# Performance work log

Measured on AMD Instinct MI355X. Metric: run time of the kernel, lower is better.

Reference implementation:

```python
import jax, jax.numpy as jnp
import numpy as np

DIM = 256
HEADS = 8
HEAD_DIM = DIM // HEADS
WS = (2, 8, 8)  # window size (t, h, w)
N = WS[0] * WS[1] * WS[2]  # 128 tokens per window
SCALE = HEAD_DIM ** -0.5
MLP_HIDDEN = int(DIM * 2.0)
EPS = 1e-5

# static relative-position index table [N, N]
def _rel_pos_index():
    coords = np.stack(np.meshgrid(np.arange(WS[0]), np.arange(WS[1]), np.arange(WS[2]), indexing='ij'))
    cf = coords.reshape(3, -1)
    rel = cf[:, :, None] - cf[:, None, :]
    rel = rel.transpose(1, 2, 0).copy()
    rel[..., 0] += WS[0] - 1
    rel[..., 1] += WS[1] - 1
    rel[..., 2] += WS[2] - 1
    rel[..., 0] *= (2 * WS[1] - 1) * (2 * WS[2] - 1)
    rel[..., 1] *= (2 * WS[2] - 1)
    return rel.sum(-1)

REL_IDX = jnp.asarray(_rel_pos_index())  # [N, N] int
TABLE_SIZE = (2 * WS[0] - 1) * (2 * WS[1] - 1) * (2 * WS[2] - 1)  # 675


def layernorm(x, g, b):
    m = jnp.mean(x, axis=-1, keepdims=True)
    var = jnp.mean(jnp.square(x - m), axis=-1, keepdims=True)
    return (x - m) * jax.lax.rsqrt(var + EPS) * g + b


def window_partition(x):
    B, T, H, W, C = x.shape
    x = x.reshape(B, T // WS[0], WS[0], H // WS[1], WS[1], W // WS[2], WS[2], C)
    x = x.transpose(0, 1, 3, 5, 2, 4, 6, 7)
    return x.reshape(-1, N, C)


def window_reverse(wins, B, T, H, W):
    C = wins.shape[-1]
    x = wins.reshape(B, T // WS[0], H // WS[1], W // WS[2], WS[0], WS[1], WS[2], C)
    x = x.transpose(0, 1, 4, 2, 5, 3, 6, 7)
    return x.reshape(B, T, H, W, C)


def setup_inputs() -> dict:
    key = jax.random.key(0)
    ks = jax.random.split(key, 20)
    B, T, H, W = 2, 8, 64, 64
    f = lambda k, s, sc=0.02: jax.random.normal(k, s, dtype=jnp.float32) * sc
    return {
        'q': jax.random.normal(ks[0], (B, T, H, W, DIM), dtype=jnp.float32),
        'k': jax.random.normal(ks[1], (B, T, H, W, DIM), dtype=jnp.float32),
        'v': jax.random.normal(ks[2], (B, T, H, W, DIM), dtype=jnp.float32),
        'gq': jnp.ones((DIM,), jnp.float32), 'bq': jnp.zeros((DIM,), jnp.float32),
        'gk': jnp.ones((DIM,), jnp.float32), 'bk': jnp.zeros((DIM,), jnp.float32),
        'gv': jnp.ones((DIM,), jnp.float32), 'bv': jnp.zeros((DIM,), jnp.float32),
        'bias_table': f(ks[3], (TABLE_SIZE, HEADS)),
        'proj_w': f(ks[4], (DIM, DIM)), 'proj_b': jnp.zeros((DIM,), jnp.float32),
        'g2': jnp.ones((DIM,), jnp.float32), 'b2': jnp.zeros((DIM,), jnp.float32),
        'mw1': f(ks[5], (MLP_HIDDEN, DIM)), 'mb1': jnp.zeros((MLP_HIDDEN,), jnp.float32),
        'mw2': f(ks[6], (DIM, MLP_HIDDEN)), 'mb2': jnp.zeros((DIM,), jnp.float32),
    }


def reference(q, k, v, gq, bq, gk, bk, gv, bv, bias_table, proj_w, proj_b, g2, b2, mw1, mb1, mw2, mb2):
    B, T, H, W, C = q.shape
    shortcut = v
    qn = layernorm(q, gq, bq)
    kn = layernorm(k, gk, bk)
    vn = layernorm(v, gv, bv)
    # (dims divisible by window -> no padding needed)
    qw = window_partition(qn)  # [B_, N, C]
    kw = window_partition(kn)
    vw = window_partition(vn)
    B_ = qw.shape[0]
    to_heads = lambda t: t.reshape(B_, N, HEADS, HEAD_DIM).transpose(0, 2, 1, 3)  # [B_, h, N, d]
    qh, kh, vh = to_heads(qw), to_heads(kw), to_heads(vw)
    attn = jnp.einsum('bhnd,bhmd->bhnm', qh * SCALE, kh)
    bias = bias_table[REL_IDX]  # [N, N, heads]
    attn = attn + bias.transpose(2, 0, 1)[None]
    attn = jax.nn.softmax(attn, axis=-1)
    out = jnp.einsum('bhnm,bhmd->bhnd', attn, vh)
    out = out.transpose(0, 2, 1, 3).reshape(B_, N, C)
    out = out @ proj_w.T + proj_b
    x = window_reverse(out, B, T, H, W)
    x = shortcut + x
    h1 = layernorm(x, g2, b2)
    h1 = jax.nn.gelu(h1 @ mw1.T + mb1, approximate=False)
    x = x + (h1 @ mw2.T + mb2)
    return x
```

## Files before the change

### kernel.cpp

```cpp
#include <hip/hip_runtime.h>
#include <math.h>


typedef __attribute__((ext_vector_type(8))) short short8;
typedef __attribute__((ext_vector_type(4))) short shortx4;
typedef __attribute__((ext_vector_type(4))) float floatx4;

#define MFMA16(a, b, c) __builtin_amdgcn_mfma_f32_16x16x32_bf16((a), (b), (c), 0, 0, 0)
#define ATT_SCALE 0.17677669529663689f

__device__ __forceinline__ short f2bf(float f) {
  unsigned u = __float_as_uint(f);
  u += 0x7fffu + ((u >> 16) & 1u);
  return (short)(u >> 16);
}
__device__ __forceinline__ float bf2f(short s) {
  return __uint_as_float(((unsigned)(unsigned short)s) << 16);
}
__device__ __forceinline__ void gl2lds(const short* g, short* l) {
  __builtin_amdgcn_global_load_lds((const __attribute__((address_space(1))) void*)(g),
                                   (__attribute__((address_space(3))) void*)(l), 16, 0, 0);
}

__global__ void cvt_kernel(const float* __restrict__ src, short* __restrict__ dst, int n) {
  int i = blockIdx.x * 256 + threadIdx.x;
  if (i < n) dst[i] = f2bf(src[i]);
}

__global__ void biasprep_kernel(const float* __restrict__ table, short* __restrict__ biasPb) {
  int idx = blockIdx.x * 256 + threadIdx.x;
  int h = idx >> 14;
  int n = (idx >> 7) & 127;
  int lr = (idx >> 3) & 15;
  int c = idx & 7;
  int m = 16 * c + lr;
  int t1 = n >> 6, h1 = (n >> 3) & 7, w1 = n & 7;
  int t2 = m >> 6, h2 = (m >> 3) & 7, w2 = m & 7;
  int ridx = (t1 - t2 + 1) * 225 + (h1 - h2 + 7) * 15 + (w1 - w2 + 7);
  biasPb[idx] = f2bf(table[ridx * 8 + h]);
}

__global__ __launch_bounds__(256) void stats_kernel(
    const float* __restrict__ q, const float* __restrict__ k, const float* __restrict__ v,
    float2* __restrict__ sq, float2* __restrict__ sk, float2* __restrict__ sv) {
  const int wv = threadIdx.x >> 6, l = threadIdx.x & 63;
  const int tok = blockIdx.x * 4 + wv;
  const int which = blockIdx.y;
  const float* src = (which == 0) ? q : ((which == 1) ? k : v);
  float2* dst = (which == 0) ? sq : ((which == 1) ? sk : sv);
  float4 xv = *(const float4*)(src + (size_t)tok * 256 + l * 4);
  float s1 = xv.x + xv.y + xv.z + xv.w;
  float s2 = xv.x * xv.x + xv.y * xv.y + xv.z * xv.z + xv.w * xv.w;
#pragma unroll
  for (int off = 1; off < 64; off <<= 1) {
    s1 += __shfl_xor(s1, off);
    s2 += __shfl_xor(s2, off);
  }
  float mean = s1 * (1.0f / 256.0f);
  float var = s2 * (1.0f / 256.0f) - mean * mean;
  if (l == 0) dst[tok] = make_float2(mean, rsqrtf(var + 1e-5f));
}

__global__ __launch_bounds__(256, 4) void attn_kernel(
    const float* __restrict__ q, const float* __restrict__ k, const float* __restrict__ v,
    const float* __restrict__ gq, const float* __restrict__ bq,
    const float* __restrict__ gk, const float* __restrict__ bk,
    const float* __restrict__ gv, const float* __restrict__ bv,
    const float2* __restrict__ sq, const float2* __restrict__ sk, const float2* __restrict__ sv,
    const short* __restrict__ biasPb, short* __restrict__ ao) {
  __shared__ union SU {
    struct { short Qs[128][40]; short Ks[128][40]; } qk;
    short Ps[128 * 128];
  } su;
  __shared__ short Vt[32 * 128];

  const int wi = blockIdx.x, h = blockIdx.y, tid = threadIdx.x;
  const int b_ = wi >> 8, tt = (wi >> 6) & 3, hb = (wi >> 3) & 7, wb = wi & 7;
  const int uu = tid & 7;

  const float4 gq4 = *(const float4*)(gq + h * 32 + uu * 4);
  const float4 bq4 = *(const float4*)(bq + h * 32 + uu * 4);
  const float4 gk4 = *(const float4*)(gk + h * 32 + uu * 4);
  const float4 bk4 = *(const float4*)(bk + h * 32 + uu * 4);
  const float4 gv4 = *(const float4*)(gv + h * 32 + uu * 4);
  const float4 bv4 = *(const float4*)(bv + h * 32 + uu * 4);

#pragma unroll
  for (int p = 0; p < 4; ++p) {
    int row = p * 32 + (tid >> 3);
    int t = row >> 6, h2 = (row >> 3) & 7, w2 = row & 7;
    size_t sidx = (((size_t)(b_ * 8 + tt * 2 + t)) * 64 + hb * 8 + h2) * 64 + wb * 8 + w2;
    size_t gbase = sidx * 256 + h * 32 + uu * 4;
    {
      float4 xv = *(const float4*)(q + gbase);
      float2 st = sq[sidx];
      shortx4 o;
      o[0] = f2bf((xv.x - st.x) * st.y * gq4.x + bq4.x);
      o[1] = f2bf((xv.y - st.x) * st.y * gq4.y + bq4.y);
      o[2] = f2bf((xv.z - st.x) * st.y * gq4.z + bq4.z);
      o[3] = f2bf((xv.w - st.x) * st.y * gq4.w + bq4.w);
      *(shortx4*)&su.qk.Qs[row][uu * 4] = o;
    }
    {
      float4 xv = *(const float4*)(k + gbase);
      float2 st = sk[sidx];
      shortx4 o;
      o[0] = f2bf((xv.x - st.x) * st.y * gk4.x + bk4.x);
      o[1] = f2bf((xv.y - st.x) * st.y * gk4.y + bk4.y);
      o[2] = f2bf((xv.z - st.x) * st.y * gk4.z + bk4.z);
      o[3] = f2bf((xv.w - st.x) * st.y * gk4.w + bk4.w);
      *(shortx4*)&su.qk.Ks[row][uu * 4] = o;
    }
    {
      float4 xv = *(const float4*)(v + gbase);
      float2 st = sv[sidx];
      float vals[4] = {(xv.x - st.x) * st.y * gv4.x + bv4.x,
                       (xv.y - st.x) * st.y * gv4.y + bv4.y,
                       (xv.z - st.x) * st.y * gv4.z + bv4.z,
                       (xv.w - st.x) * st.y * gv4.w + bv4.w};
#pragma unroll
      for (int e = 0; e < 4; ++e) {
        int d = uu * 4 + e;
        Vt[d * 128 + (((row >> 3) ^ (d & 7)) << 3) + (row & 7)] = f2bf(vals[e]);
      }
    }
  }
  __syncthreads();

  const int wvv = tid >> 6, l = tid & 63, lr = l & 15, g = l >> 4;
  const floatx4 zf = {0.f, 0.f, 0.f, 0.f};

  short8 aq0 = *(const short8*)&su.qk.Qs[32 * wvv + lr][g * 8];
  short8 aq1 = *(const short8*)&su.qk.Qs[32 * wvv + 16 + lr][g * 8];

  floatx4 s[2][8];
#pragma unroll
  for (int c = 0; c < 8; ++c) {
    short8 bk8 = *(const short8*)&su.qk.Ks[16 * c + lr][g * 8];
    s[0][c] = MFMA16(aq0, bk8, zf);
    s[1][c] = MFMA16(aq1, bk8, zf);
  }
  __syncthreads();

  const int lr7 = lr & 7;
#pragma unroll
  for (int r = 0; r < 2; ++r) {
#pragma unroll
    for (int j = 0; j < 4; ++j) {
      int n = 32 * wvv + 16 * r + 4 * g + j;
      short8 bv8 = *(const short8*)(biasPb + ((size_t)(h * 128 + n) * 16 + lr) * 8);
      float mx = -1e30f;
#pragma unroll
      for (int c = 0; c < 8; ++c) {
        float val = s[r][c][j] * ATT_SCALE + bf2f(bv8[c]);
        s[r][c][j] = val;
        mx = fmaxf(mx, val);
      }
#pragma unroll
      for (int off = 1; off < 16; off <<= 1) mx = fmaxf(mx, __shfl_xor(mx, off));
      float sum = 0.f;
#pragma unroll
      for (int c = 0; c < 8; ++c) {
        float e = __expf(s[r][c][j] - mx);
        s[r][c][j] = e;
        sum += e;
      }
#pragma unroll
      for (int off = 1; off < 16; off <<= 1) sum += __shfl_xor(sum, off);
      float invs = 1.0f / sum;
      int n7 = n & 7;
#pragma unroll
      for (int c = 0; c < 8; ++c) {
        int col = 16 * c + lr;
        su.Ps[n * 128 + (((col >> 3) ^ n7) << 3) + (col & 7)] = f2bf(s[r][c][j] * invs);
      }
    }
  }

  floatx4 o00 = zf, o01 = zf, o10 = zf, o11 = zf;
  const int ra0 = 32 * wvv + lr, ra1 = ra0 + 16;
#pragma unroll
  for (int ks = 0; ks < 4; ++ks) {
    int ulog = ks * 4 + g;
    short8 pa0 = *(const short8*)&su.Ps[ra0 * 128 + ((ulog ^ (ra0 & 7)) << 3)];
    short8 pa1 = *(const short8*)&su.Ps[ra1 * 128 + ((ulog ^ (ra1 & 7)) << 3)];
    short8 vb0 = *(const short8*)&Vt[lr * 128 + ((ulog ^ lr7) << 3)];
    short8 vb1 = *(const short8*)&Vt[(16 + lr) * 128 + ((ulog ^ lr7) << 3)];
    o00 = MFMA16(pa0, vb0, o00);
    o01 = MFMA16(pa0, vb1, o01);
    o10 = MFMA16(pa1, vb0, o10);
    o11 = MFMA16(pa1, vb1, o11);
  }
#pragma unroll
  for (int j = 0; j < 4; ++j) {
    int n0 = 32 * wvv + 4 * g + j;
    int n1 = n0 + 16;
    size_t rb0 = ((size_t)wi * 128 + n0) * 256 + h * 32;
    size_t rb1 = ((size_t)wi * 128 + n1) * 256 + h * 32;
    ao[rb0 + lr] = f2bf(o00[j]);
    ao[rb0 + 16 + lr] = f2bf(o01[j]);
    ao[rb1 + lr] = f2bf(o10[j]);
    ao[rb1 + 16 + lr] = f2bf(o11[j]);
  }
}

template <int K>
__device__ __forceinline__ void gemm_core(const short* __restrict__ A,
                                          const short* __restrict__ W,
                                          floatx4 (&acc)[16]) {
  __shared__ short As[128 * 64];
  __shared__ short Ws[256 * 64];
  const int tid = threadIdx.x;
  const int w = tid >> 6, l = tid & 63, lr = l & 15, g = l >> 4;
  const floatx4 zf = {0.f, 0.f, 0.f, 0.f};
#pragma unroll
  for (int i = 0; i < 16; ++i) acc[i] = zf;

  const int li = l >> 3, u = l & 7;
  const int swz = ((u ^ li) << 3);
  const size_t aoff0 = (size_t)(w * 8 + li) * K + swz;
  const size_t aoff1 = (size_t)((w + 8) * 8 + li) * K + swz;
  const size_t woff0 = (size_t)(w * 8 + li) * K + swz;
  const size_t woff1 = (size_t)((w + 8) * 8 + li) * K + swz;
  const size_t woff2 = (size_t)((w + 16) * 8 + li) * K + swz;
  const size_t woff3 = (size_t)((w + 24) * 8 + li) * K + swz;
  short* dA0 = As + w * 512;
  short* dA1 = As + (w + 8) * 512;
  short* dW0 = Ws + w * 512;
  short* dW1 = Ws + (w + 8) * 512;
  short* dW2 = Ws + (w + 16) * 512;
  short* dW3 = Ws + (w + 24) * 512;

  const int ra = 16 * w + lr;
  const int s0 = ((g ^ (lr & 7)) << 3);
  const int s1 = (((4 + g) ^ (lr & 7)) << 3);

  for (int k0 = 0; k0 < K; k0 += 64) {
    if (k0) __syncthreads();
    gl2lds(A + aoff0 + k0, dA0);
    gl2lds(A + aoff1 + k0, dA1);
    gl2lds(W + woff0 + k0, dW0);
    gl2lds(W + woff1 + k0, dW1);
    gl2lds(W + woff2 + k0, dW2);
    gl2lds(W + woff3 + k0, dW3);
    __syncthreads();
    short8 a0 = *(const short8*)&As[ra * 64 + s0];
    short8 a1 = *(const short8*)&As[ra * 64 + s1];
#pragma unroll
    for (int ct = 0; ct < 16; ++ct) {
      int rb = ct * 16 + lr;
      short8 b0 = *(const short8*)&Ws[rb * 64 + s0];
      acc[ct] = MFMA16(a0, b0, acc[ct]);
      short8 b1 = *(const short8*)&Ws[rb * 64 + s1];
      acc[ct] = MFMA16(a1, b1, acc[ct]);
    }
  }
}

__global__ __launch_bounds__(512, 4) void proj_kernel(
    const short* __restrict__ ao, const short* __restrict__ wp,
    const float* __restrict__ proj_b, const float* __restrict__ vin,
    const float* __restrict__ g2, const float* __restrict__ b2,
    float* __restrict__ x, short* __restrict__ xln) {
  floatx4 acc[16];
  gemm_core<256>(ao + (size_t)blockIdx.x * 128 * 256, wp, acc);
  const int tid = threadIdx.x, w = tid >> 6, l = tid & 63, lr = l & 15, g = l >> 4;
#pragma unroll
  for (int j = 0; j < 4; ++j) {
    int mrow = blockIdx.x * 128 + 16 * w + 4 * g + j;
    int wi = mrow >> 7, n = mrow & 127;
    int wb = wi & 7, hb = (wi >> 3) & 7, tt = (wi >> 6) & 3, b_ = wi >> 8;
    int t = tt * 2 + (n >> 6), hh = hb * 8 + ((n >> 3) & 7), ww = wb * 8 + (n & 7);
    size_t sidx = (((size_t)b_ * 8 + t) * 64 + hh) * 64 + ww;
    float xr[16];
    float ss1 = 0.f, ss2 = 0.f;
#pragma unroll
    for (int ct = 0; ct < 16; ++ct) {
      int col = ct * 16 + lr;
      float val = acc[ct][j] + proj_b[col] + vin[sidx * 256 + col];
      xr[ct] = val;
      ss1 += val;
      ss2 += val * val;
    }
#pragma unroll
    for (int off = 1; off < 16; off <<= 1) {
      ss1 += __shfl_xor(ss1, off);
      ss2 += __shfl_xor(ss2, off);
    }
    float mean = ss1 * (1.0f / 256.0f);
    float var = ss2 * (1.0f / 256.0f) - mean * mean;
    float inv = rsqrtf(var + 1e-5f);
#pragma unroll
    for (int ct = 0; ct < 16; ++ct) {
      int col = ct * 16 + lr;
      x[sidx * 256 + col] = xr[ct];
      xln[sidx * 256 + col] = f2bf((xr[ct] - mean) * inv * g2[col] + b2[col]);
    }
  }
}

__global__ __launch_bounds__(512, 4) void mlp1_kernel(
    const short* __restrict__ xln, const short* __restrict__ w1,
    const float* __restrict__ mb1, short* __restrict__ h1) {
  floatx4 acc[16];
  gemm_core<256>(xln + (size_t)blockIdx.x * 128 * 256, w1 + (size_t)blockIdx.y * 256 * 256, acc);
  const int tid = threadIdx.x, w = tid >> 6, l = tid & 63, lr = l & 15, g = l >> 4;
  const int colbase = blockIdx.y * 256;
#pragma unroll
  for (int ct = 0; ct < 16; ++ct) {
    int col = ct * 16 + lr;
    float bias = mb1[colbase + col];
#pragma unroll
    for (int j = 0; j < 4; ++j) {
      int mrow = blockIdx.x * 128 + 16 * w + 4 * g + j;
      float val = acc[ct][j] + bias;
      float ge = 0.5f * val * (1.0f + erff(val * 0.70710678118654752f));
      h1[(size_t)mrow * 512 + colbase + col] = f2bf(ge);
    }
  }
}

__global__ __launch_bounds__(512, 4) void mlp2_kernel(
    const short* __restrict__ h1, const short* __restrict__ w2,
    const float* __restrict__ mb2, const float* __restrict__ x,
    float* __restrict__ out) {
  floatx4 acc[16];
  gemm_core<512>(h1 + (size_t)blockIdx.x * 128 * 512, w2, acc);
  const int tid = threadIdx.x, w = tid >> 6, l = tid & 63, lr = l & 15, g = l >> 4;
#pragma unroll
  for (int ct = 0; ct < 16; ++ct) {
    int col = ct * 16 + lr;
    float bias = mb2[col];
#pragma unroll
    for (int j = 0; j < 4; ++j) {
      int mrow = blockIdx.x * 128 + 16 * w + 4 * g + j;
      out[(size_t)mrow * 256 + col] = x[(size_t)mrow * 256 + col] + acc[ct][j] + bias;
    }
  }
}

extern "C" void kernel_launch(void* const* d_in, const int* in_sizes, int n_in,
                              void* d_out, int out_size, void* d_ws, size_t ws_size,
                              hipStream_t stream) {
  const float* q = (const float*)d_in[0];
  const float* k = (const float*)d_in[1];
  const float* v = (const float*)d_in[2];
  const float* gq = (const float*)d_in[3];
  const float* bq = (const float*)d_in[4];
  const float* gk = (const float*)d_in[5];
  const float* bk = (const float*)d_in[6];
  const float* gv = (const float*)d_in[7];
  const float* bv = (const float*)d_in[8];
  const float* bias_table = (const float*)d_in[9];
  const float* proj_w = (const float*)d_in[10];
  const float* proj_b = (const float*)d_in[11];
  const float* g2 = (const float*)d_in[12];
  const float* b2 = (const float*)d_in[13];
  const float* mw1 = (const float*)d_in[14];
  const float* mb1 = (const float*)d_in[15];
  const float* mw2 = (const float*)d_in[16];
  const float* mb2 = (const float*)d_in[17];

  char* ws = (char*)d_ws;
  float2* sq = (float2*)(ws + 0);
  float2* sk = (float2*)(ws + 524288);
  float2* sv = (float2*)(ws + 1048576);
  float* x = (float*)(ws + 0);
  short* ao = (short*)(ws + 67108864);
  short* h1 = (short*)(ws + 67108864);
  short* xln = (short*)(ws + 134217728);
  short* wp = (short*)(ws + 167772160);
  short* w1 = (short*)(ws + 167903232);
  short* w2 = (short*)(ws + 168165376);
  short* biasPb = (short*)(ws + 168427520);

  cvt_kernel<<<256, 256, 0, stream>>>(proj_w, wp, 65536);
  cvt_kernel<<<512, 256, 0, stream>>>(mw1, w1, 131072);
  cvt_kernel<<<512, 256, 0, stream>>>(mw2, w2, 131072);
  biasprep_kernel<<<512, 256, 0, stream>>>(bias_table, biasPb);

  stats_kernel<<<dim3(16384, 3), 256, 0, stream>>>(q, k, v, sq, sk, sv);

  attn_kernel<<<dim3(512, 8), 256, 0, stream>>>(q, k, v, gq, bq, gk, bk, gv, bv,
                                                sq, sk, sv, biasPb, ao);

  proj_kernel<<<512, 512, 0, stream>>>(ao, wp, proj_b, v, g2, b2, x, xln);

  mlp1_kernel<<<dim3(512, 2), 512, 0, stream>>>(xln, w1, mb1, h1);

  mlp2_kernel<<<512, 512, 0, stream>>>(h1, w2, mb2, x, (float*)d_out);
}
```

Baseline: 249.5 us.

## Precompute windowed bf16 LayerNorm QKV and fuse proj+MLP into one kernel

The stats kernel now applies LayerNorm fully and writes bf16 Q/K/V already in window-partitioned order, so the attention kernel only copies contiguous bf16 tiles instead of re-reading fp32 inputs with per-head strided gathers. The projection, residual, second LayerNorm, MLP1 with GELU and MLP2 are fused into one kernel over 64-row tiles. It keeps the LN output and hidden activations in LDS and the residual in registers, which removes the global round trips for x, xln and h1. In exchange it uses heavier register and LDS use per block at lower occupancy, and reloads weights per 64-row tile.

New measurement: 236.8 us. -5.1%, faster.

```diff
diff --git a/kernel.cpp b/kernel.cpp
--- a/kernel.cpp
+++ b/kernel.cpp
@@ -40,14 +40,20 @@
   biasPb[idx] = f2bf(table[ridx * 8 + h]);
 }
 
-__global__ __launch_bounds__(256) void stats_kernel(
+__global__ __launch_bounds__(256) void ln_qkv_kernel(
     const float* __restrict__ q, const float* __restrict__ k, const float* __restrict__ v,
-    float2* __restrict__ sq, float2* __restrict__ sk, float2* __restrict__ sv) {
+    const float* __restrict__ gq, const float* __restrict__ bq,
+    const float* __restrict__ gk, const float* __restrict__ bk,
+    const float* __restrict__ gv, const float* __restrict__ bv,
+    short* __restrict__ qw, short* __restrict__ kw, short* __restrict__ vw) {
   const int wv = threadIdx.x >> 6, l = threadIdx.x & 63;
   const int tok = blockIdx.x * 4 + wv;
   const int which = blockIdx.y;
   const float* src = (which == 0) ? q : ((which == 1) ? k : v);
-  float2* dst = (which == 0) ? sq : ((which == 1) ? sk : sv);
+  const float* gg  = (which == 0) ? gq : ((which == 1) ? gk : gv);
+  const float* bb  = (which == 0) ? bq : ((which == 1) ? bk : bv);
+  short* dst       = (which == 0) ? qw : ((which == 1) ? kw : vw);
+
   float4 xv = *(const float4*)(src + (size_t)tok * 256 + l * 4);
   float s1 = xv.x + xv.y + xv.z + xv.w;
   float s2 = xv.x * xv.x + xv.y * xv.y + xv.z * xv.z + xv.w * xv.w;
@@ -58,15 +64,25 @@
   }
   float mean = s1 * (1.0f / 256.0f);
   float var = s2 * (1.0f / 256.0f) - mean * mean;
-  if (l == 0) dst[tok] = make_float2(mean, rsqrtf(var + 1e-5f));
+  float inv = rsqrtf(var + 1e-5f);
+
+  int b_ = tok >> 15, rem = tok & 32767;
+  int t = rem >> 12, hh = (rem >> 6) & 63, ww = rem & 63;
+  int wi = ((b_ * 4 + (t >> 1)) * 8 + (hh >> 3)) * 8 + (ww >> 3);
+  int n = ((t & 1) << 6) | ((hh & 7) << 3) | (ww & 7);
+
+  float4 g4 = *(const float4*)(gg + l * 4);
+  float4 b4 = *(const float4*)(bb + l * 4);
+  shortx4 o;
+  o[0] = f2bf((xv.x - mean) * inv * g4.x + b4.x);
+  o[1] = f2bf((xv.y - mean) * inv * g4.y + b4.y);
+  o[2] = f2bf((xv.z - mean) * inv * g4.z + b4.z);
+  o[3] = f2bf((xv.w - mean) * inv * g4.w + b4.w);
+  *(shortx4*)(dst + ((size_t)wi * 128 + n) * 256 + l * 4) = o;
 }
 
 __global__ __launch_bounds__(256, 4) void attn_kernel(
-    const float* __restrict__ q, const float* __restrict__ k, const float* __restrict__ v,
-    const float* __restrict__ gq, const float* __restrict__ bq,
-    const float* __restrict__ gk, const float* __restrict__ bk,
-    const float* __restrict__ gv, const float* __restrict__ bv,
-    const float2* __restrict__ sq, const float2* __restrict__ sk, const float2* __restrict__ sv,
+    const short* __restrict__ qw, const short* __restrict__ kw, const short* __restrict__ vw,
     const short* __restrict__ biasPb, short* __restrict__ ao) {
   __shared__ union SU {
     struct { short Qs[128][40]; short Ks[128][40]; } qk;
@@ -75,54 +91,19 @@
   __shared__ short Vt[32 * 128];
 
   const int wi = blockIdx.x, h = blockIdx.y, tid = threadIdx.x;
-  const int b_ = wi >> 8, tt = (wi >> 6) & 3, hb = (wi >> 3) & 7, wb = wi & 7;
-  const int uu = tid & 7;
-
-  const float4 gq4 = *(const float4*)(gq + h * 32 + uu * 4);
-  const float4 bq4 = *(const float4*)(bq + h * 32 + uu * 4);
-  const float4 gk4 = *(const float4*)(gk + h * 32 + uu * 4);
-  const float4 bk4 = *(const float4*)(bk + h * 32 + uu * 4);
-  const float4 gv4 = *(const float4*)(gv + h * 32 + uu * 4);
-  const float4 bv4 = *(const float4*)(bv + h * 32 + uu * 4);
-
-#pragma unroll
-  for (int p = 0; p < 4; ++p) {
-    int row = p * 32 + (tid >> 3);
-    int t = row >> 6, h2 = (row >> 3) & 7, w2 = row & 7;
-    size_t sidx = (((size_t)(b_ * 8 + tt * 2 + t)) * 64 + hb * 8 + h2) * 64 + wb * 8 + w2;
-    size_t gbase = sidx * 256 + h * 32 + uu * 4;
-    {
-      float4 xv = *(const float4*)(q + gbase);
-      float2 st = sq[sidx];
-      shortx4 o;
-      o[0] = f2bf((xv.x - st.x) * st.y * gq4.x + bq4.x);
-      o[1] = f2bf((xv.y - st.x) * st.y * gq4.y + bq4.y);
-      o[2] = f2bf((xv.z - st.x) * st.y * gq4.z + bq4.z);
-      o[3] = f2bf((xv.w - st.x) * st.y * gq4.w + bq4.w);
-      *(shortx4*)&su.qk.Qs[row][uu * 4] = o;
-    }
-    {
-      float4 xv = *(const float4*)(k + gbase);
-      float2 st = sk[sidx];
-      shortx4 o;
-      o[0] = f2bf((xv.x - st.x) * st.y * gk4.x + bk4.x);
-      o[1] = f2bf((xv.y - st.x) * st.y * gk4.y + bk4.y);
-      o[2] = f2bf((xv.z - st.x) * st.y * gk4.z + bk4.z);
-      o[3] = f2bf((xv.w - st.x) * st.y * gk4.w + bk4.w);
-      *(shortx4*)&su.qk.Ks[row][uu * 4] = o;
-    }
-    {
-      float4 xv = *(const float4*)(v + gbase);
-      float2 st = sv[sidx];
-      float vals[4] = {(xv.x - st.x) * st.y * gv4.x + bv4.x,
-                       (xv.y - st.x) * st.y * gv4.y + bv4.y,
-                       (xv.z - st.x) * st.y * gv4.z + bv4.z,
-                       (xv.w - st.x) * st.y * gv4.w + bv4.w};
-#pragma unroll
-      for (int e = 0; e < 4; ++e) {
-        int d = uu * 4 + e;
-        Vt[d * 128 + (((row >> 3) ^ (d & 7)) << 3) + (row & 7)] = f2bf(vals[e]);
-      }
+  const size_t base = (size_t)wi * 128 * 256 + h * 32;
+
+#pragma unroll
+  for (int i = 0; i < 2; ++i) {
+    int idx = tid + 256 * i;
+    int m = idx >> 2, c = idx & 3;
+    *(short8*)&su.qk.Qs[m][c * 8] = *(const short8*)(qw + base + (size_t)m * 256 + c * 8);
+    *(short8*)&su.qk.Ks[m][c * 8] = *(const short8*)(kw + base + (size_t)m * 256 + c * 8);
+    short8 vv = *(const short8*)(vw + base + (size_t)m * 256 + c * 8);
+#pragma unroll
+    for (int e = 0; e < 8; ++e) {
+      int d = c * 8 + e;
+      Vt[d * 128 + (((m >> 3) ^ (d & 7)) << 3) + (m & 7)] = vv[e];
     }
   }
   __syncthreads();
@@ -204,138 +185,160 @@
   }
 }
 
-template <int K>
-__device__ __forceinline__ void gemm_core(const short* __restrict__ A,
-                                          const short* __restrict__ W,
-                                          floatx4 (&acc)[16]) {
-  __shared__ short As[128 * 64];
+__global__ __launch_bounds__(256, 2) void xpath_kernel(
+    const short* __restrict__ ao, const short* __restrict__ wp,
+    const float* __restrict__ proj_b, const float* __restrict__ vin,
+    const float* __restrict__ g2, const float* __restrict__ b2,
+    const short* __restrict__ w1, const float* __restrict__ mb1,
+    const short* __restrict__ w2, const float* __restrict__ mb2,
+    float* __restrict__ out) {
   __shared__ short Ws[256 * 64];
+  __shared__ short XL[64 * 256];
+  __shared__ short H1[64 * 128];
+  short* As = H1;
+
   const int tid = threadIdx.x;
   const int w = tid >> 6, l = tid & 63, lr = l & 15, g = l >> 4;
-  const floatx4 zf = {0.f, 0.f, 0.f, 0.f};
-#pragma unroll
-  for (int i = 0; i < 16; ++i) acc[i] = zf;
-
   const int li = l >> 3, u = l & 7;
   const int swz = ((u ^ li) << 3);
-  const size_t aoff0 = (size_t)(w * 8 + li) * K + swz;
-  const size_t aoff1 = (size_t)((w + 8) * 8 + li) * K + swz;
-  const size_t woff0 = (size_t)(w * 8 + li) * K + swz;
-  const size_t woff1 = (size_t)((w + 8) * 8 + li) * K + swz;
-  const size_t woff2 = (size_t)((w + 16) * 8 + li) * K + swz;
-  const size_t woff3 = (size_t)((w + 24) * 8 + li) * K + swz;
-  short* dA0 = As + w * 512;
-  short* dA1 = As + (w + 8) * 512;
-  short* dW0 = Ws + w * 512;
-  short* dW1 = Ws + (w + 8) * 512;
-  short* dW2 = Ws + (w + 16) * 512;
-  short* dW3 = Ws + (w + 24) * 512;
-
-  const int ra = 16 * w + lr;
   const int s0 = ((g ^ (lr & 7)) << 3);
   const int s1 = (((4 + g) ^ (lr & 7)) << 3);
-
-  for (int k0 = 0; k0 < K; k0 += 64) {
+  const floatx4 zf = {0.f, 0.f, 0.f, 0.f};
+  const int bx = blockIdx.x;
+  const int r16 = 16 * w + lr;
+
+  floatx4 acc1[16];
+#pragma unroll
+  for (int i = 0; i < 16; ++i) acc1[i] = zf;
+  const short* A = ao + (size_t)bx * 64 * 256;
+  for (int k0 = 0; k0 < 256; k0 += 64) {
     if (k0) __syncthreads();
-    gl2lds(A + aoff0 + k0, dA0);
-    gl2lds(A + aoff1 + k0, dA1);
-    gl2lds(W + woff0 + k0, dW0);
-    gl2lds(W + woff1 + k0, dW1);
-    gl2lds(W + woff2 + k0, dW2);
-    gl2lds(W + woff3 + k0, dW3);
+#pragma unroll
+    for (int c = 0; c < 2; ++c)
+      gl2lds(A + (size_t)((w + 4 * c) * 8 + li) * 256 + k0 + swz, As + (w + 4 * c) * 512);
+#pragma unroll
+    for (int c = 0; c < 8; ++c)
+      gl2lds(wp + (size_t)((w + 4 * c) * 8 + li) * 256 + k0 + swz, Ws + (w + 4 * c) * 512);
     __syncthreads();
-    short8 a0 = *(const short8*)&As[ra * 64 + s0];
-    short8 a1 = *(const short8*)&As[ra * 64 + s1];
+    short8 a0 = *(const short8*)&As[r16 * 64 + s0];
+    short8 a1 = *(const short8*)&As[r16 * 64 + s1];
 #pragma unroll
     for (int ct = 0; ct < 16; ++ct) {
       int rb = ct * 16 + lr;
       short8 b0 = *(const short8*)&Ws[rb * 64 + s0];
-      acc[ct] = MFMA16(a0, b0, acc[ct]);
+      acc1[ct] = MFMA16(a0, b0, acc1[ct]);
       short8 b1 = *(const short8*)&Ws[rb * 64 + s1];
-      acc[ct] = MFMA16(a1, b1, acc[ct]);
-    }
-  }
-}
-
-__global__ __launch_bounds__(512, 4) void proj_kernel(
-    const short* __restrict__ ao, const short* __restrict__ wp,
-    const float* __restrict__ proj_b, const float* __restrict__ vin,
-    const float* __restrict__ g2, const float* __restrict__ b2,
-    float* __restrict__ x, short* __restrict__ xln) {
-  floatx4 acc[16];
-  gemm_core<256>(ao + (size_t)blockIdx.x * 128 * 256, wp, acc);
-  const int tid = threadIdx.x, w = tid >> 6, l = tid & 63, lr = l & 15, g = l >> 4;
-#pragma unroll
-  for (int j = 0; j < 4; ++j) {
-    int mrow = blockIdx.x * 128 + 16 * w + 4 * g + j;
-    int wi = mrow >> 7, n = mrow & 127;
-    int wb = wi & 7, hb = (wi >> 3) & 7, tt = (wi >> 6) & 3, b_ = wi >> 8;
-    int t = tt * 2 + (n >> 6), hh = hb * 8 + ((n >> 3) & 7), ww = wb * 8 + (n & 7);
-    size_t sidx = (((size_t)b_ * 8 + t) * 64 + hh) * 64 + ww;
-    float xr[16];
-    float ss1 = 0.f, ss2 = 0.f;
-#pragma unroll
-    for (int ct = 0; ct < 16; ++ct) {
+      acc1[ct] = MFMA16(a1, b1, acc1[ct]);
+    }
+  }
+
+  int sidx4[4];
+  float xr[16][4];
+  {
+    const int wiw = bx >> 1;
+    const int wb = wiw & 7, hb = (wiw >> 3) & 7, tt = (wiw >> 6) & 3, b_ = wiw >> 8;
+#pragma unroll
+    for (int j = 0; j < 4; ++j) {
+      int row = 16 * w + 4 * g + j;
+      int n = ((bx & 1) << 6) | row;
+      int t = tt * 2 + (n >> 6), hh = hb * 8 + ((n >> 3) & 7), ww2 = wb * 8 + (n & 7);
+      int sidx = ((b_ * 8 + t) * 64 + hh) * 64 + ww2;
+      sidx4[j] = sidx;
+      float ss1 = 0.f, ss2 = 0.f;
+#pragma unroll
+      for (int ct = 0; ct < 16; ++ct) {
+        int col = ct * 16 + lr;
+        float val = acc1[ct][j] + proj_b[col] + vin[(size_t)sidx * 256 + col];
+        xr[ct][j] = val;
+        ss1 += val;
+        ss2 += val * val;
+      }
+#pragma unroll
+      for (int off = 1; off < 16; off <<= 1) {
+        ss1 += __shfl_xor(ss1, off);
+        ss2 += __shfl_xor(ss2, off);
+      }
+      float mean = ss1 * (1.0f / 256.0f);
+      float var = ss2 * (1.0f / 256.0f) - mean * mean;
+      float inv = rsqrtf(var + 1e-5f);
+      int r7 = row & 7;
+#pragma unroll
+      for (int ct = 0; ct < 16; ++ct) {
+        int col = ct * 16 + lr;
+        float xl = (xr[ct][j] - mean) * inv * g2[col] + b2[col];
+        int uu = col >> 3;
+        XL[row * 256 + (((uu & 24) | ((uu & 7) ^ r7)) << 3) + (col & 7)] = f2bf(xl);
+      }
+    }
+  }
+  __syncthreads();
+
+  floatx4 acc3[16];
+#pragma unroll
+  for (int i = 0; i < 16; ++i) acc3[i] = zf;
+
+  for (int qt = 0; qt < 4; ++qt) {
+    floatx4 acc2[8];
+#pragma unroll
+    for (int i = 0; i < 8; ++i) acc2[i] = zf;
+    for (int k0 = 0; k0 < 256; k0 += 64) {
+      __syncthreads();
+#pragma unroll
+      for (int c = 0; c < 4; ++c)
+        gl2lds(w1 + (size_t)(qt * 128 + (w + 4 * c) * 8 + li) * 256 + k0 + swz,
+               Ws + (w + 4 * c) * 512);
+      __syncthreads();
+      short8 a0 = *(const short8*)&XL[r16 * 256 + k0 + ((g ^ (r16 & 7)) << 3)];
+      short8 a1 = *(const short8*)&XL[r16 * 256 + k0 + (((4 + g) ^ (r16 & 7)) << 3)];
+#pragma unroll
+      for (int ct = 0; ct < 8; ++ct) {
+        int rb = ct * 16 + lr;
+        short8 b0 = *(const short8*)&Ws[rb * 64 + s0];
+        acc2[ct] = MFMA16(a0, b0, acc2[ct]);
+        short8 b1 = *(const short8*)&Ws[rb * 64 + s1];
+        acc2[ct] = MFMA16(a1, b1, acc2[ct]);
+      }
+    }
+#pragma unroll
+    for (int ct = 0; ct < 8; ++ct) {
       int col = ct * 16 + lr;
-      float val = acc[ct][j] + proj_b[col] + vin[sidx * 256 + col];
-      xr[ct] = val;
-      ss1 += val;
-      ss2 += val * val;
-    }
-#pragma unroll
-    for (int off = 1; off < 16; off <<= 1) {
-      ss1 += __shfl_xor(ss1, off);
-      ss2 += __shfl_xor(ss2, off);
-    }
-    float mean = ss1 * (1.0f / 256.0f);
-    float var = ss2 * (1.0f / 256.0f) - mean * mean;
-    float inv = rsqrtf(var + 1e-5f);
-#pragma unroll
-    for (int ct = 0; ct < 16; ++ct) {
-      int col = ct * 16 + lr;
-      x[sidx * 256 + col] = xr[ct];
-      xln[sidx * 256 + col] = f2bf((xr[ct] - mean) * inv * g2[col] + b2[col]);
-    }
-  }
-}
-
-__global__ __launch_bounds__(512, 4) void mlp1_kernel(
-    const short* __restrict__ xln, const short* __restrict__ w1,
-    const float* __restrict__ mb1, short* __restrict__ h1) {
-  floatx4 acc[16];
-  gemm_core<256>(xln + (size_t)blockIdx.x * 128 * 256, w1 + (size_t)blockIdx.y * 256 * 256, acc);
-  const int tid = threadIdx.x, w = tid >> 6, l = tid & 63, lr = l & 15, g = l >> 4;
-  const int colbase = blockIdx.y * 256;
-#pragma unroll
-  for (int ct = 0; ct < 16; ++ct) {
-    int col = ct * 16 + lr;
-    float bias = mb1[colbase + col];
-#pragma unroll
-    for (int j = 0; j < 4; ++j) {
-      int mrow = blockIdx.x * 128 + 16 * w + 4 * g + j;
-      float val = acc[ct][j] + bias;
-      float ge = 0.5f * val * (1.0f + erff(val * 0.70710678118654752f));
-      h1[(size_t)mrow * 512 + colbase + col] = f2bf(ge);
-    }
-  }
-}
-
-__global__ __launch_bounds__(512, 4) void mlp2_kernel(
-    const short* __restrict__ h1, const short* __restrict__ w2,
-    const float* __restrict__ mb2, const float* __restrict__ x,
-    float* __restrict__ out) {
-  floatx4 acc[16];
-  gemm_core<512>(h1 + (size_t)blockIdx.x * 128 * 512, w2, acc);
-  const int tid = threadIdx.x, w = tid >> 6, l = tid & 63, lr = l & 15, g = l >> 4;
+      float bias = mb1[qt * 128 + col];
+#pragma unroll
+      for (int j = 0; j < 4; ++j) {
+        int row = 16 * w + 4 * g + j;
+        float val = acc2[ct][j] + bias;
+        float ge = 0.5f * val * (1.0f + erff(val * 0.70710678118654752f));
+        int uu = col >> 3;
+        H1[row * 128 + (((uu & 8) | ((uu & 7) ^ (row & 7))) << 3) + (col & 7)] = f2bf(ge);
+      }
+    }
+    for (int k0 = 0; k0 < 128; k0 += 64) {
+      __syncthreads();
+#pragma unroll
+      for (int c = 0; c < 8; ++c)
+        gl2lds(w2 + (size_t)((w + 4 * c) * 8 + li) * 512 + qt * 128 + k0 + swz,
+               Ws + (w + 4 * c) * 512);
+      __syncthreads();
+      short8 a0 = *(const short8*)&H1[r16 * 128 + k0 + ((g ^ (r16 & 7)) << 3)];
+      short8 a1 = *(const short8*)&H1[r16 * 128 + k0 + (((4 + g) ^ (r16 & 7)) << 3)];
+#pragma unroll
+      for (int ct = 0; ct < 16; ++ct) {
+        int rb = ct * 16 + lr;
+        short8 b0 = *(const short8*)&Ws[rb * 64 + s0];
+        acc3[ct] = MFMA16(a0, b0, acc3[ct]);
+        short8 b1 = *(const short8*)&Ws[rb * 64 + s1];
+        acc3[ct] = MFMA16(a1, b1, acc3[ct]);
+      }
+    }
+  }
+
 #pragma unroll
   for (int ct = 0; ct < 16; ++ct) {
     int col = ct * 16 + lr;
     float bias = mb2[col];
 #pragma unroll
-    for (int j = 0; j < 4; ++j) {
-      int mrow = blockIdx.x * 128 + 16 * w + 4 * g + j;
-      out[(size_t)mrow * 256 + col] = x[(size_t)mrow * 256 + col] + acc[ct][j] + bias;
-    }
+    for (int j = 0; j < 4; ++j)
+      out[(size_t)sidx4[j] * 256 + col] = xr[ct][j] + acc3[ct][j] + bias;
   }
 }
 
@@ -362,13 +365,10 @@
   const float* mb2 = (const float*)d_in[17];
 
   char* ws = (char*)d_ws;
-  float2* sq = (float2*)(ws + 0);
-  float2* sk = (float2*)(ws + 524288);
-  float2* sv = (float2*)(ws + 1048576);
-  float* x = (float*)(ws + 0);
-  short* ao = (short*)(ws + 67108864);
-  short* h1 = (short*)(ws + 67108864);
-  short* xln = (short*)(ws + 134217728);
+  short* qw = (short*)(ws + 0);
+  short* kw = (short*)(ws + 33554432);
+  short* vw = (short*)(ws + 67108864);
+  short* ao = (short*)(ws + 100663296);
   short* wp = (short*)(ws + 167772160);
   short* w1 = (short*)(ws + 167903232);
   short* w2 = (short*)(ws + 168165376);
@@ -379,14 +379,10 @@
   cvt_kernel<<<512, 256, 0, stream>>>(mw2, w2, 131072);
   biasprep_kernel<<<512, 256, 0, stream>>>(bias_table, biasPb);
 
-  stats_kernel<<<dim3(16384, 3), 256, 0, stream>>>(q, k, v, sq, sk, sv);
-
-  attn_kernel<<<dim3(512, 8), 256, 0, stream>>>(q, k, v, gq, bq, gk, bk, gv, bv,
-                                                sq, sk, sv, biasPb, ao);
-
-  proj_kernel<<<512, 512, 0, stream>>>(ao, wp, proj_b, v, g2, b2, x, xln);
-
-  mlp1_kernel<<<dim3(512, 2), 512, 0, stream>>>(xln, w1, mb1, h1);
-
-  mlp2_kernel<<<512, 512, 0, stream>>>(h1, w2, mb2, x, (float*)d_out);
-}
+  ln_qkv_kernel<<<dim3(16384, 3), 256, 0, stream>>>(q, k, v, gq, bq, gk, bk, gv, bv, qw, kw, vw);
+
+  attn_kernel<<<dim3(512, 8), 256, 0, stream>>>(qw, kw, vw, biasPb, ao);
+
+  xpath_kernel<<<1024, 256, 0, stream>>>(ao, wp, proj_b, v, g2, b2, w1, mb1, w2, mb2,
+                                         (float*)d_out);
+}
```
